# Kernel tuning notes

Measured on AMD Instinct MI355X. Metric: run time of the kernel, lower is better.

The kernel has to match this reference:

```python
import jax, jax.numpy as jnp
import numpy as np

NEG = -1e9  # max-semiring 'zero' / structural mask value


def _cky_max(pot, lengths):
    """Max-plus CKY inside pass (torch_struct CKY_CRF with MaxSemiring).

    pot: [B, N, N] label-maxed span potentials, pot[b, i, j] = score of span (i, j).
    Returns [B] best binary-tree score for each sequence of given length.
    betaA[b, i, w]      = best score of span starting at i with width w (span [i, i+w]).
    betaB[b, j, N-1-w]  = best score of span ending at j with width w.
    """
    B, N, _ = pot.shape
    term = jnp.diagonal(pot, axis1=1, axis2=2)  # [B, N] width-0 spans
    betaA = jnp.full((B, N, N), NEG, dtype=pot.dtype).at[:, :, 0].set(term)
    betaB = jnp.full((B, N, N), NEG, dtype=pot.dtype).at[:, :, N - 1].set(term)
    for w in range(1, N):
        Y = betaA[:, : N - w, :w]       # [B, N-w, w] left children, widths 0..w-1
        Z = betaB[:, w:, N - w:]        # [B, N-w, w] right children (matching splits)
        span = jnp.diagonal(pot, offset=w, axis1=1, axis2=2)  # [B, N-w] pot[b, i, i+w]
        new = jnp.max(Y + Z, axis=-1) + span
        betaA = betaA.at[:, : N - w, w].set(new)
        betaB = betaB.at[:, w:, N - w - 1].set(new)
    final = betaA[:, 0, :]  # [B, N]: final[b, l-1] = best tree over [0, l-1]
    return final[jnp.arange(B), lengths - 1]


def setup_inputs() -> dict:
    key = jax.random.key(0)
    k1, k2 = jax.random.split(key)
    B, N, L = 64, 128, 32
    logits = jax.random.normal(k1, (B, N, N, L), dtype=jnp.float32)
    labels = jax.random.randint(k2, (B, N, N), 0, L, dtype=jnp.int64)
    return {"logits": logits, "labels": labels}


def reference(logits, labels):
    B, N, _, L = logits.shape
    gold_event = jax.nn.one_hot(jnp.maximum(labels, 0), L, dtype=logits.dtype)
    logits = logits - logits[..., :1]
    lengths = jnp.sum(labels[:, 0, :] != -100, axis=-1)
    augment = 1.0 - gold_event
    # force_root_constituent=True: forbid non-constituent root span
    augment = augment.at[jnp.arange(B), 0, lengths - 1, 0].add(-1e9)
    pot = jnp.max(logits + augment, axis=-1)  # max-semiring sum over label dim
    pred_score = _cky_max(pot, lengths)                      # [B]
    gold_score = jnp.sum(logits * gold_event, axis=(1, 2, 3))  # [B]
    margin_losses = jax.nn.relu(pred_score - gold_score)
    return jnp.mean(margin_losses)
```

## Files before the change

kernel.cpp:

```cpp
#include <hip/hip_runtime.h>

#define BATCH 64
#define SEQ   128
#define NLAB  32
#define NEGF  -3.0e38f
#define PA    132

__global__ __launch_bounds__(256) void pot_gold_kernel(
    const float* __restrict__ logits, const int* __restrict__ labels,
    float* __restrict__ pot, float* __restrict__ gpart)
{
    const int tid = threadIdx.x;
    const int wave = tid >> 6, lane = tid & 63;
    __shared__ __align__(16) float LP[4 * 16 * 36];
    __shared__ float gred[4];
    __shared__ int s_len;
    float* W = LP + wave * (16 * 36);

    const int block_cell0 = blockIdx.x * 256;
    const int b = block_cell0 >> 14;
    const bool has_row0 = (blockIdx.x & 63) == 0;

    if (has_row0 && tid < 64) {
        const size_t base = (size_t)b << 14;
        int cnt = (labels[base + tid] != -100) + (labels[base + 64 + tid] != -100);
        #pragma unroll
        for (int d = 32; d; d >>= 1) cnt += __shfl_down(cnt, d, 64);
        if (tid == 0) s_len = cnt;
    }
    __syncthreads();
    const int len = has_row0 ? s_len : -1;

    float gacc = 0.0f;
    const int wave_cell0 = block_cell0 + wave * 64;

    #pragma unroll
    for (int chunk = 0; chunk < 4; ++chunk) {
        const int c0 = wave_cell0 + chunk * 16;
        const float4* src = reinterpret_cast<const float4*>(logits) + ((size_t)c0 << 3);
        const float4 f0 = src[lane];
        const float4 f1 = src[lane + 64];
        const int lv = (lane < 16) ? labels[c0 + lane] : 0;

        {
            const int cA = lane >> 3, tA = lane & 7;
            *reinterpret_cast<float4*>(W + cA * 36 + tA * 4) = f0;
            const int q1 = lane + 64;
            const int cB = q1 >> 3, tB = q1 & 7;
            *reinterpret_cast<float4*>(W + cB * 36 + tB * 4) = f1;
        }
        const int c = lane >> 2, u = lane & 3;
        const float4 r0 = *reinterpret_cast<const float4*>(W + c * 36 + u * 8);
        const float4 r1 = *reinterpret_cast<const float4*>(W + c * 36 + u * 8 + 4);

        int lab = __shfl(lv, c, 64);
        if (lab < 0) lab = 0;
        const float l0 = __shfl(r0.x, c << 2, 64);

        const int cell = c0 + c;
        const int ci = (cell >> 7) & (SEQ - 1);
        const int cj = cell & (SEQ - 1);
        const bool special = (ci == 0) && (cj == len - 1);

        const float vv[8] = { r0.x, r0.y, r0.z, r0.w, r1.x, r1.y, r1.z, r1.w };
        float m = NEGF, g = 0.0f;
        #pragma unroll
        for (int e = 0; e < 8; ++e) {
            const int l = u * 8 + e;
            const float r = vv[e] - l0;
            const bool isg = (l == lab);
            g = isg ? r : g;
            float cand = r + (isg ? 0.0f : 1.0f);
            if (l == 0 && special) cand -= 1.0e9f;
            m = fmaxf(m, cand);
        }
        m = fmaxf(m, __shfl_xor(m, 1, 64));
        m = fmaxf(m, __shfl_xor(m, 2, 64));
        g += __shfl_xor(g, 1, 64);
        g += __shfl_xor(g, 2, 64);
        if (u == 0) {
            pot[cell] = m;
            gacc += g;
        }
    }

    #pragma unroll
    for (int d = 1; d < 64; d <<= 1) gacc += __shfl_xor(gacc, d, 64);
    if (lane == 0) gred[wave] = gacc;
    __syncthreads();
    if (tid == 0)
        gpart[blockIdx.x] = gred[0] + gred[1] + gred[2] + gred[3];
}

__global__ __launch_bounds__(512, 1) void cky_kernel(
    const float* __restrict__ pot, const float* __restrict__ gpart,
    const int* __restrict__ labels, float* __restrict__ out)
{
    const int b = blockIdx.x;
    const int tid = threadIdx.x;
    const float* p = pot + (size_t)b * SEQ * SEQ;

    __shared__ __align__(16) float A[SEQ * PA];
    __shared__ __align__(16) float Bt[SEQ * PA];
    __shared__ int s_len;
    __shared__ float s_gold;

    if (tid < 64) {
        const size_t base = (size_t)b << 14;
        int cnt = (labels[base + tid] != -100) + (labels[base + 64 + tid] != -100);
        #pragma unroll
        for (int d = 32; d; d >>= 1) cnt += __shfl_down(cnt, d, 64);
        if (tid == 0) s_len = cnt;
    } else if (tid < 128) {
        float g = gpart[b * 64 + (tid - 64)];
        #pragma unroll
        for (int d = 32; d; d >>= 1) g += __shfl_down(g, d, 64);
        if (tid == 64) s_gold = g;
    }

    {
        const float4* p4 = reinterpret_cast<const float4*>(p);
        for (int qi = tid; qi < SEQ * SEQ / 4; qi += 512) {
            const int i = qi >> 5;
            const int j0 = (qi & 31) << 2;
            const float4 v = p4[qi];
            const float vv[4] = { v.x, v.y, v.z, v.w };
            #pragma unroll
            for (int c2 = 0; c2 < 4; ++c2) {
                const int j = j0 + c2;
                if (j >= i) {
                    A[i * PA + (j - i)] = vv[c2];
                    Bt[j * PA + (SEQ - 1 - (j - i))] = vv[c2];
                }
            }
        }
    }
    __syncthreads();

    const int i = tid >> 2, s = tid & 3;
    float alo[16], av[16], pv[16], md[16];

    #pragma unroll
    for (int t = 0; t < 4; ++t) {
        const float4 v = *reinterpret_cast<const float4*>(&A[i * PA + 4 * t]);
        pv[4*t] = v.x; pv[4*t+1] = v.y; pv[4*t+2] = v.z; pv[4*t+3] = v.w;
    }
    av[0] = pv[0];
    #pragma unroll
    for (int d = 1; d < 16; ++d) {
        const int j = i + d;
        if (j < SEQ) {
            float bo[16];
            const int NQ = (d + 3) >> 2;
            #pragma unroll
            for (int t = 0; t < NQ; ++t) {
                const float4 v = *reinterpret_cast<const float4*>(&Bt[j * PA + 124 - 4 * t]);
                bo[4*t] = v.w; bo[4*t+1] = v.z; bo[4*t+2] = v.y; bo[4*t+3] = v.x;
            }
            float val = NEGF;
            #pragma unroll
            for (int m = 0; m < d; ++m)
                val = fmaxf(val, av[d - 1 - m] + bo[m]);
            val += pv[d];
            av[d] = val;
            if (s == 0) {
                A[i * PA + d] = val;
                Bt[j * PA + (SEQ - 1 - d)] = val;
            }
        }
        __syncthreads();
    }
    #pragma unroll
    for (int k = 0; k < 16; ++k) alo[k] = av[k];

    for (int W = 16; W < SEQ; W += 16) {
        #pragma unroll
        for (int t = 0; t < 4; ++t) {
            const float4 v = *reinterpret_cast<const float4*>(&A[i * PA + W + 4 * t]);
            pv[4*t] = v.x; pv[4*t+1] = v.y; pv[4*t+2] = v.z; pv[4*t+3] = v.w;
        }
        #pragma unroll
        for (int d = 0; d < 16; ++d) md[d] = NEGF;

        {
            const int k0 = s << 2;
            const float4 a = *reinterpret_cast<const float4*>(&A[i * PA + k0]);
            const float aa[4] = { a.x, a.y, a.z, a.w };
            #pragma unroll
            for (int d = 0; d < 16; ++d) {
                const int j = i + W + d;
                if (j < SEQ) {
                    const float* bp = &Bt[j * PA + (SEQ - W - d) + k0];
                    float b0, b1, b2, b3;
                    if ((d & 3) == 0) {
                        const float4 v = *reinterpret_cast<const float4*>(bp);
                        b0 = v.x; b1 = v.y; b2 = v.z; b3 = v.w;
                    } else if ((d & 3) == 2) {
                        const float2 v0 = *reinterpret_cast<const float2*>(bp);
                        const float2 v1 = *reinterpret_cast<const float2*>(bp + 2);
                        b0 = v0.x; b1 = v0.y; b2 = v1.x; b3 = v1.y;
                    } else {
                        b0 = bp[0];
                        const float2 v = *reinterpret_cast<const float2*>(bp + 1);
                        b1 = v.x; b2 = v.y; b3 = bp[3];
                    }
                    const float a0 = (k0 + 0 >= d) ? aa[0] : NEGF;
                    const float a1 = (k0 + 1 >= d) ? aa[1] : NEGF;
                    const float a2 = (k0 + 2 >= d) ? aa[2] : NEGF;
                    const float a3 = (k0 + 3 >= d) ? aa[3] : NEGF;
                    md[d] = fmaxf(md[d], fmaxf(fmaxf(a0 + b0, a1 + b1),
                                               fmaxf(a2 + b2, a3 + b3)));
                }
            }
        }
        for (int q = s + 4; q < (W >> 2); q += 4) {
            const int k0 = q << 2;
            const float4 a = *reinterpret_cast<const float4*>(&A[i * PA + k0]);
            #pragma unroll
            for (int d = 0; d < 16; ++d) {
                const int j = i + W + d;
                if (j < SEQ) {
                    const float* bp = &Bt[j * PA + (SEQ - W - d) + k0];
                    float b0, b1, b2, b3;
                    if ((d & 3) == 0) {
                        const float4 v = *reinterpret_cast<const float4*>(bp);
                        b0 = v.x; b1 = v.y; b2 = v.z; b3 = v.w;
                    } else if ((d & 3) == 2) {
                        const float2 v0 = *reinterpret_cast<const float2*>(bp);
                        const float2 v1 = *reinterpret_cast<const float2*>(bp + 2);
                        b0 = v0.x; b1 = v0.y; b2 = v1.x; b3 = v1.y;
                    } else {
                        b0 = bp[0];
                        const float2 v = *reinterpret_cast<const float2*>(bp + 1);
                        b1 = v.x; b2 = v.y; b3 = bp[3];
                    }
                    md[d] = fmaxf(md[d], fmaxf(fmaxf(a.x + b0, a.y + b1),
                                               fmaxf(a.z + b2, a.w + b3)));
                }
            }
        }
        #pragma unroll
        for (int d = 0; d < 16; ++d) {
            md[d] = fmaxf(md[d], __shfl_xor(md[d], 1, 4));
            md[d] = fmaxf(md[d], __shfl_xor(md[d], 2, 4));
        }

        #pragma unroll
        for (int d = 0; d < 16; ++d) {
            const int w = W + d;
            const int j = i + w;
            if (j < SEQ) {
                float val = md[d];
                if (d > 0) {
                    float bo[16], bf[16];
                    const int NQ = (d + 3) >> 2;
                    #pragma unroll
                    for (int t = 0; t < NQ; ++t) {
                        const float4 v = *reinterpret_cast<const float4*>(&Bt[j * PA + 124 - 4 * t]);
                        bo[4*t] = v.w; bo[4*t+1] = v.z; bo[4*t+2] = v.y; bo[4*t+3] = v.x;
                        const float4 u = *reinterpret_cast<const float4*>(&Bt[j * PA + 124 - W - 4 * t]);
                        bf[4*t] = u.w; bf[4*t+1] = u.z; bf[4*t+2] = u.y; bf[4*t+3] = u.x;
                    }
                    #pragma unroll
                    for (int m = 0; m < d; ++m) {
                        val = fmaxf(val, av[d - 1 - m] + bo[m]);
                        val = fmaxf(val, alo[d - 1 - m] + bf[m]);
                    }
                }
                val += pv[d];
                av[d] = val;
                if (s == 0) {
                    A[i * PA + w] = val;
                    Bt[j * PA + (SEQ - 1 - w)] = val;
                }
            }
            __syncthreads();
        }
    }

    if (tid == 0) {
        const int len = s_len;
        const float pred = A[len - 1];
        const float margin = fmaxf(pred - s_gold, 0.0f);
        atomicAdd(out, margin * (1.0f / (float)BATCH));
    }
}

extern "C" void kernel_launch(void* const* d_in, const int* in_sizes, int n_in,
                              void* d_out, int out_size, void* d_ws, size_t ws_size,
                              hipStream_t stream) {
    const float* logits = (const float*)d_in[0];
    const int* labels = (const int*)d_in[1];
    float* out = (float*)d_out;

    float* pot = (float*)d_ws;
    float* gpart = pot + (size_t)BATCH * SEQ * SEQ;

    (void)hipMemsetAsync(out, 0, sizeof(float), stream);

    pot_gold_kernel<<<BATCH * SEQ * SEQ / 256, 256, 0, stream>>>(
        logits, labels, pot, gpart);
    cky_kernel<<<BATCH, 512, 0, stream>>>(pot, gpart, labels, out);
}
```

Before: 258.5 us.

## Prefetch next-diagonal LDS operands across barriers, tree-reduce max, and drop memset

The serial CKY diagonal loop now issues the LDS loads for the next width's already-finalized right-child values before the barrier, using a partial lgkmcnt wait so only the newest value has to be read after synchronization. The per-cell max becomes a balanced tree instead of a linear chain, which shortens the dependency chain on the critical path. The pot staging load is unrolled so all global loads are in flight together, and the output memset is folded into the first kernel, removing one launch. The hand-written waitcnt counts depend on exact compiler instruction ordering, so a mismatch could cause races. The memset folding relies on the first kernel finishing before the second kernel's atomics, which holds for in-order stream execution.

```diff
diff --git a/kernel.cpp b/kernel.cpp
--- a/kernel.cpp
+++ b/kernel.cpp
@@ -6,9 +6,23 @@
 #define NEGF  -3.0e38f
 #define PA    132
 
+__device__ __forceinline__ void bar_k(int K) {
+    switch (K) {
+    case 0: asm volatile("s_waitcnt lgkmcnt(0)" ::: "memory"); break;
+    case 1: asm volatile("s_waitcnt lgkmcnt(1)" ::: "memory"); break;
+    case 2: asm volatile("s_waitcnt lgkmcnt(2)" ::: "memory"); break;
+    case 3: asm volatile("s_waitcnt lgkmcnt(3)" ::: "memory"); break;
+    case 4: asm volatile("s_waitcnt lgkmcnt(4)" ::: "memory"); break;
+    case 5: asm volatile("s_waitcnt lgkmcnt(5)" ::: "memory"); break;
+    case 6: asm volatile("s_waitcnt lgkmcnt(6)" ::: "memory"); break;
+    default: asm volatile("s_waitcnt lgkmcnt(7)" ::: "memory"); break;
+    }
+    __builtin_amdgcn_s_barrier();
+}
+
 __global__ __launch_bounds__(256) void pot_gold_kernel(
     const float* __restrict__ logits, const int* __restrict__ labels,
-    float* __restrict__ pot, float* __restrict__ gpart)
+    float* __restrict__ pot, float* __restrict__ gpart, float* __restrict__ out)
 {
     const int tid = threadIdx.x;
     const int wave = tid >> 6, lane = tid & 63;
@@ -20,6 +34,8 @@
     const int block_cell0 = blockIdx.x * 256;
     const int b = block_cell0 >> 14;
     const bool has_row0 = (blockIdx.x & 63) == 0;
+
+    if (blockIdx.x == 0 && tid == 0) out[0] = 0.0f;
 
     if (has_row0 && tid < 64) {
         const size_t base = (size_t)b << 14;
@@ -120,17 +136,21 @@
 
     {
         const float4* p4 = reinterpret_cast<const float4*>(p);
-        for (int qi = tid; qi < SEQ * SEQ / 4; qi += 512) {
-            const int i = qi >> 5;
+        float4 vb[8];
+        #pragma unroll
+        for (int t = 0; t < 8; ++t) vb[t] = p4[tid + 512 * t];
+        #pragma unroll
+        for (int t = 0; t < 8; ++t) {
+            const int qi = tid + 512 * t;
+            const int i0 = qi >> 5;
             const int j0 = (qi & 31) << 2;
-            const float4 v = p4[qi];
-            const float vv[4] = { v.x, v.y, v.z, v.w };
+            const float vv[4] = { vb[t].x, vb[t].y, vb[t].z, vb[t].w };
             #pragma unroll
             for (int c2 = 0; c2 < 4; ++c2) {
                 const int j = j0 + c2;
-                if (j >= i) {
-                    A[i * PA + (j - i)] = vv[c2];
-                    Bt[j * PA + (SEQ - 1 - (j - i))] = vv[c2];
+                if (j >= i0) {
+                    A[i0 * PA + (j - i0)] = vv[c2];
+                    Bt[j * PA + (SEQ - 1 - (j - i0))] = vv[c2];
                 }
             }
         }
@@ -139,6 +159,7 @@
 
     const int i = tid >> 2, s = tid & 3;
     float alo[16], av[16], pv[16], md[16];
+    float bo_p[16], bf_p[12];
 
     #pragma unroll
     for (int t = 0; t < 4; ++t) {
@@ -149,26 +170,44 @@
     #pragma unroll
     for (int d = 1; d < 16; ++d) {
         const int j = i + d;
-        if (j < SEQ) {
-            float bo[16];
-            const int NQ = (d + 3) >> 2;
-            #pragma unroll
-            for (int t = 0; t < NQ; ++t) {
-                const float4 v = *reinterpret_cast<const float4*>(&Bt[j * PA + 124 - 4 * t]);
-                bo[4*t] = v.w; bo[4*t+1] = v.z; bo[4*t+2] = v.y; bo[4*t+3] = v.x;
-            }
-            float val = NEGF;
-            #pragma unroll
-            for (int m = 0; m < d; ++m)
-                val = fmaxf(val, av[d - 1 - m] + bo[m]);
-            val += pv[d];
-            av[d] = val;
-            if (s == 0) {
-                A[i * PA + d] = val;
-                Bt[j * PA + (SEQ - 1 - d)] = val;
-            }
-        }
-        __syncthreads();
+        const int tf = (d - 1) >> 2;
+        const int jr = (j < SEQ) ? j : SEQ - 1;
+        float bff[4];
+        {
+            const float4 u = *reinterpret_cast<const float4*>(&Bt[jr * PA + 124 - 4 * tf]);
+            bff[0] = u.w; bff[1] = u.z; bff[2] = u.y; bff[3] = u.x;
+        }
+        float e[16];
+        #pragma unroll
+        for (int m = 0; m < d; ++m)
+            e[m] = av[d - 1 - m] + ((m < 4 * tf) ? bo_p[m] : bff[m - 4 * tf]);
+        #pragma unroll
+        for (int stp = 1; stp < 16; stp <<= 1) {
+            #pragma unroll
+            for (int m = 0; m + stp < d; m += 2 * stp)
+                e[m] = fmaxf(e[m], e[m + stp]);
+        }
+        const float val = e[0] + pv[d];
+        av[d] = val;
+        if (j < SEQ && s == 0) {
+            A[i * PA + d] = val;
+            Bt[j * PA + (SEQ - 1 - d)] = val;
+        }
+        __builtin_amdgcn_sched_barrier(0);
+        if (d < 15) {
+            int jp = j + 1; if (jp >= SEQ) jp = SEQ - 1;
+            const int tfn = d >> 2;
+            #pragma unroll
+            for (int t = 0; t < 4; ++t) {
+                if (t < tfn) {
+                    const float4 v = *reinterpret_cast<const float4*>(&Bt[jp * PA + 124 - 4 * t]);
+                    bo_p[4*t] = v.w; bo_p[4*t+1] = v.z; bo_p[4*t+2] = v.y; bo_p[4*t+3] = v.x;
+                }
+            }
+            bar_k(tfn);
+        } else {
+            bar_k(0);
+        }
     }
     #pragma unroll
     for (int k = 0; k < 16; ++k) alo[k] = av[k];
@@ -245,36 +284,73 @@
             md[d] = fmaxf(md[d], __shfl_xor(md[d], 2, 4));
         }
 
-        #pragma unroll
-        for (int d = 0; d < 16; ++d) {
+        {
+            const int j = i + W;
+            const float val = md[0] + pv[0];
+            av[0] = val;
+            if (j < SEQ && s == 0) {
+                A[i * PA + W] = val;
+                Bt[j * PA + (SEQ - 1 - W)] = val;
+            }
+            __builtin_amdgcn_sched_barrier(0);
+            int jp = j + 1; if (jp >= SEQ) jp = SEQ - 1;
+            const float4 v = *reinterpret_cast<const float4*>(&Bt[jp * PA + 124]);
+            bo_p[0] = v.w; bo_p[1] = v.z; bo_p[2] = v.y; bo_p[3] = v.x;
+            bar_k(1);
+        }
+        #pragma unroll
+        for (int d = 1; d < 16; ++d) {
             const int w = W + d;
             const int j = i + w;
-            if (j < SEQ) {
-                float val = md[d];
-                if (d > 0) {
-                    float bo[16], bf[16];
-                    const int NQ = (d + 3) >> 2;
-                    #pragma unroll
-                    for (int t = 0; t < NQ; ++t) {
-                        const float4 v = *reinterpret_cast<const float4*>(&Bt[j * PA + 124 - 4 * t]);
-                        bo[4*t] = v.w; bo[4*t+1] = v.z; bo[4*t+2] = v.y; bo[4*t+3] = v.x;
-                        const float4 u = *reinterpret_cast<const float4*>(&Bt[j * PA + 124 - W - 4 * t]);
-                        bf[4*t] = u.w; bf[4*t+1] = u.z; bf[4*t+2] = u.y; bf[4*t+3] = u.x;
+            const int tf = (d - 1) >> 2;
+            const int jr = (j < SEQ) ? j : SEQ - 1;
+            float bff[4];
+            {
+                const float4 u = *reinterpret_cast<const float4*>(&Bt[jr * PA + 124 - W - 4 * tf]);
+                bff[0] = u.w; bff[1] = u.z; bff[2] = u.y; bff[3] = u.x;
+            }
+            float e[30];
+            #pragma unroll
+            for (int m = 0; m < d; ++m)
+                e[m] = av[d - 1 - m] + bo_p[m];
+            #pragma unroll
+            for (int m = 0; m < d; ++m)
+                e[d + m] = alo[d - 1 - m] + ((m < 4 * tf) ? bf_p[m] : bff[m - 4 * tf]);
+            #pragma unroll
+            for (int stp = 1; stp < 32; stp <<= 1) {
+                #pragma unroll
+                for (int m = 0; m + stp < 2 * d; m += 2 * stp)
+                    e[m] = fmaxf(e[m], e[m + stp]);
+            }
+            const float val = fmaxf(md[d], e[0]) + pv[d];
+            av[d] = val;
+            if (j < SEQ && s == 0) {
+                A[i * PA + w] = val;
+                Bt[j * PA + (SEQ - 1 - w)] = val;
+            }
+            __builtin_amdgcn_sched_barrier(0);
+            if (d < 15) {
+                int jp = j + 1; if (jp >= SEQ) jp = SEQ - 1;
+                const int NQn = (d + 4) >> 2;
+                #pragma unroll
+                for (int t = 0; t < 4; ++t) {
+                    if (t < NQn) {
+                        const float4 v = *reinterpret_cast<const float4*>(&Bt[jp * PA + 124 - 4 * t]);
+                        bo_p[4*t] = v.w; bo_p[4*t+1] = v.z; bo_p[4*t+2] = v.y; bo_p[4*t+3] = v.x;
                     }
-                    #pragma unroll
-                    for (int m = 0; m < d; ++m) {
-                        val = fmaxf(val, av[d - 1 - m] + bo[m]);
-                        val = fmaxf(val, alo[d - 1 - m] + bf[m]);
+                }
+                const int tfn = d >> 2;
+                #pragma unroll
+                for (int t = 0; t < 3; ++t) {
+                    if (t < tfn) {
+                        const float4 v = *reinterpret_cast<const float4*>(&Bt[jp * PA + 124 - W - 4 * t]);
+                        bf_p[4*t] = v.w; bf_p[4*t+1] = v.z; bf_p[4*t+2] = v.y; bf_p[4*t+3] = v.x;
                     }
                 }
-                val += pv[d];
-                av[d] = val;
-                if (s == 0) {
-                    A[i * PA + w] = val;
-                    Bt[j * PA + (SEQ - 1 - w)] = val;
-                }
-            }
-            __syncthreads();
+                bar_k(NQn + tfn);
+            } else {
+                bar_k(0);
+            }
         }
     }
 
@@ -296,9 +372,7 @@
     float* pot = (float*)d_ws;
     float* gpart = pot + (size_t)BATCH * SEQ * SEQ;
 
-    (void)hipMemsetAsync(out, 0, sizeof(float), stream);
-
     pot_gold_kernel<<<BATCH * SEQ * SEQ / 256, 256, 0, stream>>>(
-        logits, labels, pot, gpart);
+        logits, labels, pot, gpart, out);
     cky_kernel<<<BATCH, 512, 0, stream>>>(pot, gpart, labels, out);
 }
```

After: 258.0 us. No clear change (-0.2%).
